# Kernel optimization log

Hardware: AMD Instinct MI355X
Metric: run time of the kernel (lower is better)

## Reference

```python
import jax, jax.numpy as jnp
from jax import lax
import numpy as np

N, V, P, WE, PE, H, M = 512, 50000, 50, 100, 25, 256, 100
D = WE + PE  # 125, LSTM layer-0 input


def setup_inputs() -> dict:
    key = jax.random.key(0)
    ks = jax.random.split(key, 16)
    s = 0.05  # keep tanh/sigmoid in linear-ish range
    rn = lambda k, shape: jax.random.normal(k, shape, jnp.float32) * s
    return {
        "word_idx": jax.random.randint(ks[0], (N,), 0, V),
        "pos_idx": jax.random.randint(ks[1], (N,), 0, P),
        "word_emb": rn(ks[2], (V, WE)),
        "pos_emb": rn(ks[3], (P, PE)),
        "Wih0": rn(ks[4], (2, 4 * H, D)),
        "Whh0": rn(ks[5], (2, 4 * H, H)),
        "bih0": rn(ks[6], (2, 4 * H)),
        "bhh0": rn(ks[7], (2, 4 * H)),
        "Wih1": rn(ks[8], (2, 4 * H, 2 * H)),
        "Whh1": rn(ks[9], (2, 4 * H, H)),
        "bih1": rn(ks[10], (2, 4 * H)),
        "bhh1": rn(ks[11], (2, 4 * H)),
        "W1": rn(ks[12], (M, 4 * H)),
        "b1": rn(ks[13], (M,)),
        "W2": rn(ks[14], (1, M)),
        "b2": rn(ks[15], (1,)),
    }


def _lstm_dir(x, Wih, Whh, bih, bhh, reverse):
    # x: [n, d_in]; PyTorch gate order i, f, g, o
    Hh = Whh.shape[1]
    xp = jnp.flip(x, 0) if reverse else x
    pre = xp @ Wih.T + (bih + bhh)  # [n, 4H], input contribution precomputed

    def step(carry, p):
        h, c = carry
        g = p + h @ Whh.T
        i, f, gg, o = jnp.split(g, 4)
        c = jax.nn.sigmoid(f) * c + jax.nn.sigmoid(i) * jnp.tanh(gg)
        h = jax.nn.sigmoid(o) * jnp.tanh(c)
        return (h, c), h

    init = (jnp.zeros((Hh,), x.dtype), jnp.zeros((Hh,), x.dtype))
    _, hs = lax.scan(step, init, pre)
    return jnp.flip(hs, 0) if reverse else hs


def _bilstm_layer(x, Wih, Whh, bih, bhh):
    fwd = _lstm_dir(x, Wih[0], Whh[0], bih[0], bhh[0], False)
    bwd = _lstm_dir(x, Wih[1], Whh[1], bih[1], bhh[1], True)
    return jnp.concatenate([fwd, bwd], axis=-1)  # [n, 2H]


def reference(word_idx, pos_idx, word_emb, pos_emb,
              Wih0, Whh0, bih0, bhh0, Wih1, Whh1, bih1, bhh1,
              W1, b1, W2, b2):
    # embedding lookup + concat -> [n, D]
    embeds = jnp.concatenate([word_emb[word_idx], pos_emb[pos_idx]], axis=-1)
    h = _bilstm_layer(embeds, Wih0, Whh0, bih0, bhh0)   # [n, 2H]
    h = _bilstm_layer(h, Wih1, Whh1, bih1, bhh1)        # [n, 2H]
    # Pairwise MLP scorer: score[i, j] = W2 @ tanh(W1 @ cat(h_i, h_j) + b1) + b2
    # Split W1 so we never materialize the [n, n, 4H] concat tensor.
    Hd = h.shape[-1]
    a = h @ W1[:, :Hd].T   # [n, M] head part
    b = h @ W1[:, Hd:].T   # [n, M] dep part
    hid = jnp.tanh(a[:, None, :] + b[None, :, :] + b1)  # [n, n, M]
    scores = jnp.einsum('ijm,m->ij', hid, W2[0]) + b2[0]
    return scores
```

## Files before the change

### kernel.cpp

```cpp
#include <hip/hip_runtime.h>
#include <hip/hip_bf16.h>
#include <stdint.h>


typedef _Float16 f16x2 __attribute__((ext_vector_type(2)));

#define SCOPE_AGENT __HIP_MEMORY_SCOPE_AGENT
constexpr uint32_t SENT = 0x7FFF7FFFu;

__device__ __forceinline__ float fdot2f(uint32_t w, uint32_t h, float acc) {
#if __has_builtin(__builtin_amdgcn_fdot2)
  return __builtin_amdgcn_fdot2(__builtin_bit_cast(f16x2, w),
                                __builtin_bit_cast(f16x2, h), acc, false);
#else
  f16x2 a = __builtin_bit_cast(f16x2, w);
  f16x2 b = __builtin_bit_cast(f16x2, h);
  return acc + (float)a.x * (float)b.x + (float)a.y * (float)b.y;
#endif
}

__device__ __forceinline__ float fsigm(float x) { return 1.f / (1.f + __expf(-x)); }
__device__ __forceinline__ float ftanh(float x) {
  float e = __expf(2.f * x);
  return 1.f - 2.f / (e + 1.f);
}

constexpr size_t ALN(size_t x) { return (x + 1023) & ~(size_t)1023; }
constexpr size_t O_EX    = 0;
constexpr size_t SZ_EX   = 4ull * 512 * 128 * 4;
constexpr size_t O_WPK   = ALN(O_EX + SZ_EX);
constexpr size_t SZ_WPK  = 4ull * 128 * 1024 * 4;
constexpr size_t O_X0    = ALN(O_WPK + SZ_WPK);
constexpr size_t SZ_X0   = 512ull * 125 * 4;
constexpr size_t O_WTIH0 = ALN(O_X0 + SZ_X0);
constexpr size_t SZ_WTIH0 = 2ull * 128 * 1024 * 4;
constexpr size_t O_WTIH1 = ALN(O_WTIH0 + SZ_WTIH0);
constexpr size_t SZ_WTIH1 = 2ull * 512 * 1024 * 4;
constexpr size_t O_WTA   = ALN(O_WTIH1 + SZ_WTIH1);
constexpr size_t SZ_WTAB = 512ull * 100 * 4;
constexpr size_t O_WTB   = ALN(O_WTA + SZ_WTAB);
constexpr size_t O_PRE0  = ALN(O_WTB + SZ_WTAB);
constexpr size_t SZ_PRE  = 2ull * 512 * 1024 * 4;
constexpr size_t O_PRE1  = ALN(O_PRE0 + SZ_PRE);
constexpr size_t O_H0    = ALN(O_PRE1 + SZ_PRE);
constexpr size_t SZ_H    = 512ull * 512 * 4;
constexpr size_t O_H1    = ALN(O_H0 + SZ_H);
constexpr size_t O_AM    = ALN(O_H1 + SZ_H);
constexpr size_t O_BT    = ALN(O_AM + SZ_WTAB);


__global__ void k_init_ex(uint32_t* __restrict__ ex) {
  ex[(size_t)blockIdx.x * 256 + threadIdx.x] = SENT;
}

__global__ void k_embed(const int* __restrict__ wi, const int* __restrict__ pi,
                        const float* __restrict__ we, const float* __restrict__ pe,
                        float* __restrict__ x0) {
  int i = blockIdx.x, k = threadIdx.x;
  if (k < 100)      x0[i * 125 + k] = we[(size_t)wi[i] * 100 + k];
  else if (k < 125) x0[i * 125 + k] = pe[(size_t)pi[i] * 25 + (k - 100)];
}

__global__ void k_transpose(const float* __restrict__ src, int srcRows, int srcCols,
                            int colOff, int colCnt, int dstRows, float* __restrict__ dst) {
  __shared__ float tile[32][33];
  int k0 = blockIdx.x * 32, m0 = blockIdx.y * 32;
  int tx = threadIdx.x, ty = threadIdx.y;
#pragma unroll
  for (int i = 0; i < 4; i++) {
    int m = m0 + ty + i * 8, k = k0 + tx;
    float v = 0.f;
    if (m < srcRows && k < colCnt) v = src[(size_t)m * srcCols + colOff + k];
    tile[ty + i * 8][tx] = v;
  }
  __syncthreads();
#pragma unroll
  for (int i = 0; i < 4; i++) {
    int k = k0 + ty + i * 8, m = m0 + tx;
    if (k < dstRows && m < srcRows) dst[(size_t)k * srcRows + m] = tile[tx][ty + i * 8];
  }
}

__global__ void k_packwhh(const float* __restrict__ whh0, const float* __restrict__ whh1,
                          uint32_t* __restrict__ wpk) {
  int ld = blockIdx.x;
  int kp = blockIdx.y;
  int o  = threadIdx.x;
  const float* W = (ld < 2) ? (whh0 + (size_t)ld * 1024 * 256)
                            : (whh1 + (size_t)(ld - 2) * 1024 * 256);
  int b = o >> 9, t = o & 511;
  int gate = t >> 7, u = t & 127;
  int R = gate * 256 + b * 128 + u;
  f16x2 p;
  p.x = (_Float16)W[(size_t)R * 256 + 2 * kp];
  p.y = (_Float16)W[(size_t)R * 256 + 2 * kp + 1];
  wpk[(size_t)ld * 131072 + (size_t)(kp >> 2) * 4096 + (size_t)o * 4 + (kp & 3)] =
      __builtin_bit_cast(uint32_t, p);
}

__global__ __launch_bounds__(256) void k_gemm(
    const float* __restrict__ X, const float* __restrict__ WT,
    const float* __restrict__ bias1, const float* __restrict__ bias2,
    float* __restrict__ out, int Mm, int Nn, int Kpad, int Kreal, int ldx,
    int flipX, int outT) {
  __shared__ float XS[32][64];
  int tid = threadIdx.x;
  int cl = tid & 63, rg = tid >> 6;
  int col = blockIdx.y * 64 + cl;
  int colr = (col < Nn) ? col : (Nn - 1);
  int row0 = blockIdx.x * 32;
  float acc[8];
#pragma unroll
  for (int r = 0; r < 8; r++) acc[r] = 0.f;
  for (int k0 = 0; k0 < Kpad; k0 += 64) {
#pragma unroll
    for (int ii = 0; ii < 8; ii++) {
      int idx = ii * 256 + tid;
      int r = idx >> 6, kk = idx & 63;
      int gr = row0 + r;
      int xr = flipX ? (Mm - 1 - gr) : gr;
      int k = k0 + kk;
      XS[r][kk] = (k < Kreal) ? X[(size_t)xr * ldx + k] : 0.f;
    }
    __syncthreads();
#pragma unroll 4
    for (int kk = 0; kk < 64; kk++) {
      float w = WT[(size_t)(k0 + kk) * Nn + colr];
#pragma unroll
      for (int r = 0; r < 8; r++) acc[r] += XS[rg * 8 + r][kk] * w;
    }
    __syncthreads();
  }
  if (col < Nn) {
    float bb = (bias1 ? bias1[col] : 0.f) + (bias2 ? bias2[col] : 0.f);
#pragma unroll
    for (int r = 0; r < 8; r++) {
      int gr = row0 + rg * 8 + r;
      float v = acc[r] + bb;
      if (outT) out[(size_t)col * Mm + gr] = v;
      else      out[(size_t)gr * Nn + col] = v;
    }
  }
}

__global__ __launch_bounds__(512, 2) void k_lstm(
    const float* __restrict__ preBase, const uint32_t* __restrict__ wpkL,
    float* __restrict__ hout, uint32_t* __restrict__ exL) {
  int d = blockIdx.x >> 1, b = blockIdx.x & 1;
  int t = threadIdx.x;
  const float* pre = preBase + (size_t)d * 512 * 1024;
  const uint32_t* wsrc = wpkL + (size_t)d * 131072;
  uint32_t* ex = exL + (size_t)d * 512 * 128;

  __shared__ __align__(16) uint32_t h2[128];
  __shared__ __align__(8) float gl[512];

  const uint4* wv = (const uint4*)wsrc;
  const int o = b * 512 + t;
#define WLOAD(i) uint4 W##i = wv[(i) * 1024 + o];
  WLOAD(0)  WLOAD(1)  WLOAD(2)  WLOAD(3)  WLOAD(4)  WLOAD(5)  WLOAD(6)  WLOAD(7)
  WLOAD(8)  WLOAD(9)  WLOAD(10) WLOAD(11) WLOAD(12) WLOAD(13) WLOAD(14) WLOAD(15)
  WLOAD(16) WLOAD(17) WLOAD(18) WLOAD(19) WLOAD(20) WLOAD(21) WLOAD(22) WLOAD(23)
  WLOAD(24) WLOAD(25) WLOAD(26) WLOAD(27) WLOAD(28) WLOAD(29) WLOAD(30) WLOAD(31)
#undef WLOAD
#define WPIN(i) asm volatile("" : "+v"(W##i.x), "+v"(W##i.y), "+v"(W##i.z), "+v"(W##i.w));
  WPIN(0)  WPIN(1)  WPIN(2)  WPIN(3)  WPIN(4)  WPIN(5)  WPIN(6)  WPIN(7)
  WPIN(8)  WPIN(9)  WPIN(10) WPIN(11) WPIN(12) WPIN(13) WPIN(14) WPIN(15)
  WPIN(16) WPIN(17) WPIN(18) WPIN(19) WPIN(20) WPIN(21) WPIN(22) WPIN(23)
  WPIN(24) WPIN(25) WPIN(26) WPIN(27) WPIN(28) WPIN(29) WPIN(30) WPIN(31)
#undef WPIN

  if (t < 128) h2[t] = 0u;
  float c0 = 0.f, c1 = 0.f;
  const int gate = t >> 7, u = t & 127;
  const int RR = gate * 256 + b * 128 + u;
  __syncthreads();

  float pcur = pre[RR];
  for (int s = 0; s < 512; s++) {
    float pnext = (s < 511) ? pre[(size_t)(s + 1) * 1024 + RR] : 0.f;
    float a0 = pcur, a1 = 0.f, a2 = 0.f, a3 = 0.f;
    const uint4* h4 = (const uint4*)h2;
#define DOT(i) { uint4 hv = h4[i];                 \
      a0 = fdot2f(W##i.x, hv.x, a0);               \
      a1 = fdot2f(W##i.y, hv.y, a1);               \
      a2 = fdot2f(W##i.z, hv.z, a2);               \
      a3 = fdot2f(W##i.w, hv.w, a3); }
    DOT(0)  DOT(1)  DOT(2)  DOT(3)  DOT(4)  DOT(5)  DOT(6)  DOT(7)
    DOT(8)  DOT(9)  DOT(10) DOT(11) DOT(12) DOT(13) DOT(14) DOT(15)
    DOT(16) DOT(17) DOT(18) DOT(19) DOT(20) DOT(21) DOT(22) DOT(23)
    DOT(24) DOT(25) DOT(26) DOT(27) DOT(28) DOT(29) DOT(30) DOT(31)
#undef DOT
    gl[t] = (a0 + a1) + (a2 + a3);
    __syncthreads();
    if (t < 64) {
      const float2* GL2 = (const float2*)gl;
      float2 gi = GL2[t];
      float2 gf = GL2[64 + t];
      float2 gg = GL2[128 + t];
      float2 go = GL2[192 + t];
      c0 = fsigm(gf.x) * c0 + fsigm(gi.x) * ftanh(gg.x);
      c1 = fsigm(gf.y) * c1 + fsigm(gi.y) * ftanh(gg.y);
      float hA = fsigm(go.x) * ftanh(c0);
      float hB = fsigm(go.y) * ftanh(c1);
      f16x2 p;
      p.x = (_Float16)hA;
      p.y = (_Float16)hB;
      uint32_t pk = __builtin_bit_cast(uint32_t, p);
      __hip_atomic_store(&ex[(size_t)s * 128 + b * 64 + t], pk,
                         __ATOMIC_RELAXED, SCOPE_AGENT);
      h2[b * 64 + t] = pk;
      int pos = (d == 0) ? s : (511 - s);
      *(float2*)&hout[(size_t)pos * 512 + d * 256 + b * 128 + 2 * t] =
          make_float2(hA, hB);
    } else if (t < 128) {
      int tt = t - 64;
      uint32_t q;
      do {
        q = __hip_atomic_load(&ex[(size_t)s * 128 + (b ^ 1) * 64 + tt],
                              __ATOMIC_RELAXED, SCOPE_AGENT);
      } while (__any(q == SENT));
      h2[(b ^ 1) * 64 + tt] = q;
    }
    pcur = pnext;
    __syncthreads();
  }
}

__global__ __launch_bounds__(512) void k_score(
    const float* __restrict__ am, const float* __restrict__ bT,
    const float* __restrict__ W2, const float* __restrict__ b2,
    float* __restrict__ out) {
  int i = blockIdx.x;
  int j = threadIdx.x;
  __shared__ float aL[100], w2L[100];
  if (j < 100) { aL[j] = am[(size_t)i * 100 + j]; w2L[j] = W2[j]; }
  __syncthreads();
  float acc = b2[0];
#pragma unroll 4
  for (int m = 0; m < 100; m++)
    acc += w2L[m] * ftanh(aL[m] + bT[(size_t)m * 512 + j]);
  out[(size_t)i * 512 + j] = acc;
}

extern "C" void kernel_launch(void* const* d_in, const int* in_sizes, int n_in,
                              void* d_out, int out_size, void* d_ws, size_t ws_size,
                              hipStream_t stream) {
  const int*   wi   = (const int*)d_in[0];
  const int*   pi   = (const int*)d_in[1];
  const float* we   = (const float*)d_in[2];
  const float* pe   = (const float*)d_in[3];
  const float* Wih0 = (const float*)d_in[4];
  const float* Whh0 = (const float*)d_in[5];
  const float* bih0 = (const float*)d_in[6];
  const float* bhh0 = (const float*)d_in[7];
  const float* Wih1 = (const float*)d_in[8];
  const float* Whh1 = (const float*)d_in[9];
  const float* bih1 = (const float*)d_in[10];
  const float* bhh1 = (const float*)d_in[11];
  const float* W1   = (const float*)d_in[12];
  const float* b1   = (const float*)d_in[13];
  const float* W2   = (const float*)d_in[14];
  const float* b2   = (const float*)d_in[15];

  char* ws = (char*)d_ws;
  uint32_t* ex    = (uint32_t*)(ws + O_EX);
  uint32_t* wpk   = (uint32_t*)(ws + O_WPK);
  float* x0    = (float*)(ws + O_X0);
  float* wtih0 = (float*)(ws + O_WTIH0);
  float* wtih1 = (float*)(ws + O_WTIH1);
  float* wta   = (float*)(ws + O_WTA);
  float* wtb   = (float*)(ws + O_WTB);
  float* pre0  = (float*)(ws + O_PRE0);
  float* pre1  = (float*)(ws + O_PRE1);
  float* h0    = (float*)(ws + O_H0);
  float* h1    = (float*)(ws + O_H1);
  float* am    = (float*)(ws + O_AM);
  float* bt    = (float*)(ws + O_BT);
  float* out   = (float*)d_out;

  k_init_ex<<<1024, 256, 0, stream>>>(ex);

  k_embed<<<512, 128, 0, stream>>>(wi, pi, we, pe, x0);

  dim3 tb(32, 8);
  k_transpose<<<dim3(4, 32),  tb, 0, stream>>>(Wih0,              1024, 125, 0,   125, 128, wtih0);
  k_transpose<<<dim3(4, 32),  tb, 0, stream>>>(Wih0 + 1024 * 125, 1024, 125, 0,   125, 128, wtih0 + 128 * 1024);
  k_transpose<<<dim3(16, 32), tb, 0, stream>>>(Wih1,              1024, 512, 0,   512, 512, wtih1);
  k_transpose<<<dim3(16, 32), tb, 0, stream>>>(Wih1 + 1024 * 512, 1024, 512, 0,   512, 512, wtih1 + 512 * 1024);
  k_transpose<<<dim3(16, 4),  tb, 0, stream>>>(W1,                100, 1024, 0,   512, 512, wta);
  k_transpose<<<dim3(16, 4),  tb, 0, stream>>>(W1,                100, 1024, 512, 512, 512, wtb);

  k_packwhh<<<dim3(4, 128), 1024, 0, stream>>>(Whh0, Whh1, wpk);

  for (int d = 0; d < 2; d++)
    k_gemm<<<dim3(16, 16), 256, 0, stream>>>(x0, wtih0 + (size_t)d * 128 * 1024,
        bih0 + d * 1024, bhh0 + d * 1024, pre0 + (size_t)d * 512 * 1024,
        512, 1024, 128, 125, 125, d, 0);

  k_lstm<<<4, 512, 0, stream>>>(pre0, wpk, h0, ex);

  for (int d = 0; d < 2; d++)
    k_gemm<<<dim3(16, 16), 256, 0, stream>>>(h0, wtih1 + (size_t)d * 512 * 1024,
        bih1 + d * 1024, bhh1 + d * 1024, pre1 + (size_t)d * 512 * 1024,
        512, 1024, 512, 512, 512, d, 0);

  k_lstm<<<4, 512, 0, stream>>>(pre1, wpk + 2 * 131072, h1, ex + 2ull * 512 * 128);

  k_gemm<<<dim3(16, 2), 256, 0, stream>>>(h1, wta, b1, nullptr, am, 512, 100, 512, 512, 512, 0, 0);
  k_gemm<<<dim3(16, 2), 256, 0, stream>>>(h1, wtb, nullptr, nullptr, bt, 512, 100, 512, 512, 512, 0, 1);

  k_score<<<512, 512, 0, stream>>>(am, bt, W2, b2, out);
}
```

Before: 2.735 ms.

## Split LSTM recurrent dot-product K dimension across two half-blocks of 1024 threads

```diff
diff --git a/kernel.cpp b/kernel.cpp
--- a/kernel.cpp
+++ b/kernel.cpp
@@ -19,6 +19,13 @@
 #endif
 }
 
+__device__ __forceinline__ uint32_t packpair(float x, float y) {
+  f16x2 p;
+  p.x = (_Float16)x;
+  p.y = (_Float16)y;
+  return __builtin_bit_cast(uint32_t, p);
+}
+
 __device__ __forceinline__ float fsigm(float x) { return 1.f / (1.f + __expf(-x)); }
 __device__ __forceinline__ float ftanh(float x) {
   float e = __expf(2.f * x);
@@ -29,7 +36,7 @@
 constexpr size_t O_EX    = 0;
 constexpr size_t SZ_EX   = 4ull * 512 * 128 * 4;
 constexpr size_t O_WPK   = ALN(O_EX + SZ_EX);
-constexpr size_t SZ_WPK  = 4ull * 128 * 1024 * 4;
+constexpr size_t SZ_WPK  = 4ull * 16 * 2048 * 16;
 constexpr size_t O_X0    = ALN(O_WPK + SZ_WPK);
 constexpr size_t SZ_X0   = 512ull * 125 * 4;
 constexpr size_t O_WTIH0 = ALN(O_X0 + SZ_X0);
@@ -84,18 +91,22 @@
 __global__ void k_packwhh(const float* __restrict__ whh0, const float* __restrict__ whh1,
                           uint32_t* __restrict__ wpk) {
   int ld = blockIdx.x;
-  int kp = blockIdx.y;
-  int o  = threadIdx.x;
+  int c  = blockIdx.y;
+  int o  = blockIdx.z * 1024 + threadIdx.x;
   const float* W = (ld < 2) ? (whh0 + (size_t)ld * 1024 * 256)
                             : (whh1 + (size_t)(ld - 2) * 1024 * 256);
-  int b = o >> 9, t = o & 511;
-  int gate = t >> 7, u = t & 127;
+  int b = o >> 10, t = o & 1023;
+  int hi = t >> 9, tr = t & 511;
+  int gate = tr >> 7, u = tr & 127;
   int R = gate * 256 + b * 128 + u;
-  f16x2 p;
-  p.x = (_Float16)W[(size_t)R * 256 + 2 * kp];
-  p.y = (_Float16)W[(size_t)R * 256 + 2 * kp + 1];
-  wpk[(size_t)ld * 131072 + (size_t)(kp >> 2) * 4096 + (size_t)o * 4 + (kp & 3)] =
-      __builtin_bit_cast(uint32_t, p);
+  int khalf = hi ? (b ^ 1) : b;
+  const float* src = W + (size_t)R * 256 + khalf * 128 + c * 8;
+  uint4 outv;
+  outv.x = packpair(src[0], src[1]);
+  outv.y = packpair(src[2], src[3]);
+  outv.z = packpair(src[4], src[5]);
+  outv.w = packpair(src[6], src[7]);
+  ((uint4*)wpk)[(size_t)ld * 32768 + (size_t)c * 2048 + o] = outv;
 }
 
 __global__ __launch_bounds__(256) void k_gemm(
@@ -143,70 +154,67 @@
   }
 }
 
-__global__ __launch_bounds__(512, 2) void k_lstm(
+__global__ __launch_bounds__(1024) void k_lstm(
     const float* __restrict__ preBase, const uint32_t* __restrict__ wpkL,
     float* __restrict__ hout, uint32_t* __restrict__ exL) {
   int d = blockIdx.x >> 1, b = blockIdx.x & 1;
   int t = threadIdx.x;
+  int tr = t & 511, hi = t >> 9;
   const float* pre = preBase + (size_t)d * 512 * 1024;
-  const uint32_t* wsrc = wpkL + (size_t)d * 131072;
   uint32_t* ex = exL + (size_t)d * 512 * 128;
+  const uint4* wv = (const uint4*)(wpkL + (size_t)d * 131072);
 
   __shared__ __align__(16) uint32_t h2[128];
-  __shared__ __align__(8) float gl[512];
-
-  const uint4* wv = (const uint4*)wsrc;
-  const int o = b * 512 + t;
-#define WLOAD(i) uint4 W##i = wv[(i) * 1024 + o];
+  __shared__ __align__(8) float shp[1024];
+
+  const int o = b * 1024 + t;
+  const int khalf = hi ? (b ^ 1) : b;
+
+#define WLOAD(i) uint4 W##i = wv[(i) * 2048 + o];
   WLOAD(0)  WLOAD(1)  WLOAD(2)  WLOAD(3)  WLOAD(4)  WLOAD(5)  WLOAD(6)  WLOAD(7)
   WLOAD(8)  WLOAD(9)  WLOAD(10) WLOAD(11) WLOAD(12) WLOAD(13) WLOAD(14) WLOAD(15)
-  WLOAD(16) WLOAD(17) WLOAD(18) WLOAD(19) WLOAD(20) WLOAD(21) WLOAD(22) WLOAD(23)
-  WLOAD(24) WLOAD(25) WLOAD(26) WLOAD(27) WLOAD(28) WLOAD(29) WLOAD(30) WLOAD(31)
 #undef WLOAD
 #define WPIN(i) asm volatile("" : "+v"(W##i.x), "+v"(W##i.y), "+v"(W##i.z), "+v"(W##i.w));
   WPIN(0)  WPIN(1)  WPIN(2)  WPIN(3)  WPIN(4)  WPIN(5)  WPIN(6)  WPIN(7)
   WPIN(8)  WPIN(9)  WPIN(10) WPIN(11) WPIN(12) WPIN(13) WPIN(14) WPIN(15)
-  WPIN(16) WPIN(17) WPIN(18) WPIN(19) WPIN(20) WPIN(21) WPIN(22) WPIN(23)
-  WPIN(24) WPIN(25) WPIN(26) WPIN(27) WPIN(28) WPIN(29) WPIN(30) WPIN(31)
 #undef WPIN
 
   if (t < 128) h2[t] = 0u;
   float c0 = 0.f, c1 = 0.f;
-  const int gate = t >> 7, u = t & 127;
+  const int gate = tr >> 7, u = tr & 127;
   const int RR = gate * 256 + b * 128 + u;
+  float pcur = (t < 512) ? pre[RR] : 0.f;
   __syncthreads();
 
-  float pcur = pre[RR];
   for (int s = 0; s < 512; s++) {
-    float pnext = (s < 511) ? pre[(size_t)(s + 1) * 1024 + RR] : 0.f;
+    float pnext = (t < 512 && s < 511) ? pre[(size_t)(s + 1) * 1024 + RR] : 0.f;
     float a0 = pcur, a1 = 0.f, a2 = 0.f, a3 = 0.f;
-    const uint4* h4 = (const uint4*)h2;
-#define DOT(i) { uint4 hv = h4[i];                 \
+    const uint4* hb = ((const uint4*)h2) + khalf * 16;
+#define DOT(i) { uint4 hv = hb[i];                 \
       a0 = fdot2f(W##i.x, hv.x, a0);               \
       a1 = fdot2f(W##i.y, hv.y, a1);               \
       a2 = fdot2f(W##i.z, hv.z, a2);               \
       a3 = fdot2f(W##i.w, hv.w, a3); }
     DOT(0)  DOT(1)  DOT(2)  DOT(3)  DOT(4)  DOT(5)  DOT(6)  DOT(7)
     DOT(8)  DOT(9)  DOT(10) DOT(11) DOT(12) DOT(13) DOT(14) DOT(15)
-    DOT(16) DOT(17) DOT(18) DOT(19) DOT(20) DOT(21) DOT(22) DOT(23)
-    DOT(24) DOT(25) DOT(26) DOT(27) DOT(28) DOT(29) DOT(30) DOT(31)
 #undef DOT
-    gl[t] = (a0 + a1) + (a2 + a3);
+    shp[t] = (a0 + a1) + (a2 + a3);
     __syncthreads();
     if (t < 64) {
-      const float2* GL2 = (const float2*)gl;
-      float2 gi = GL2[t];
-      float2 gf = GL2[64 + t];
-      float2 gg = GL2[128 + t];
-      float2 go = GL2[192 + t];
-      c0 = fsigm(gf.x) * c0 + fsigm(gi.x) * ftanh(gg.x);
-      c1 = fsigm(gf.y) * c1 + fsigm(gi.y) * ftanh(gg.y);
-      float hA = fsigm(go.x) * ftanh(c0);
-      float hB = fsigm(go.y) * ftanh(c1);
-      f16x2 p;
-      p.x = (_Float16)hA;
-      p.y = (_Float16)hB;
-      uint32_t pk = __builtin_bit_cast(uint32_t, p);
+      const float2* SP2 = (const float2*)shp;
+      float2 giA = SP2[t],       giB = SP2[256 + t];
+      float2 gfA = SP2[64 + t],  gfB = SP2[320 + t];
+      float2 ggA = SP2[128 + t], ggB = SP2[384 + t];
+      float2 goA = SP2[192 + t], goB = SP2[448 + t];
+      float gi0 = giA.x + giB.x, gi1 = giA.y + giB.y;
+      float gf0 = gfA.x + gfB.x, gf1 = gfA.y + gfB.y;
+      float gg0 = ggA.x + ggB.x, gg1 = ggA.y + ggB.y;
+      float go0 = goA.x + goB.x, go1 = goA.y + goB.y;
+      c0 = fsigm(gf0) * c0 + fsigm(gi0) * ftanh(gg0);
+      c1 = fsigm(gf1) * c1 + fsigm(gi1) * ftanh(gg1);
+      float hA = fsigm(go0) * ftanh(c0);
+      float hB = fsigm(go1) * ftanh(c1);
+      uint32_t pk = packpair(hA, hB);
       __hip_atomic_store(&ex[(size_t)s * 128 + b * 64 + t], pk,
                          __ATOMIC_RELAXED, SCOPE_AGENT);
       h2[b * 64 + t] = pk;
@@ -291,21 +299,21 @@
   k_transpose<<<dim3(16, 4),  tb, 0, stream>>>(W1,                100, 1024, 0,   512, 512, wta);
   k_transpose<<<dim3(16, 4),  tb, 0, stream>>>(W1,                100, 1024, 512, 512, 512, wtb);
 
-  k_packwhh<<<dim3(4, 128), 1024, 0, stream>>>(Whh0, Whh1, wpk);
+  k_packwhh<<<dim3(4, 16, 2), 1024, 0, stream>>>(Whh0, Whh1, wpk);
 
   for (int d = 0; d < 2; d++)
     k_gemm<<<dim3(16, 16), 256, 0, stream>>>(x0, wtih0 + (size_t)d * 128 * 1024,
         bih0 + d * 1024, bhh0 + d * 1024, pre0 + (size_t)d * 512 * 1024,
         512, 1024, 128, 125, 125, d, 0);
 
-  k_lstm<<<4, 512, 0, stream>>>(pre0, wpk, h0, ex);
+  k_lstm<<<4, 1024, 0, stream>>>(pre0, wpk, h0, ex);
 
   for (int d = 0; d < 2; d++)
     k_gemm<<<dim3(16, 16), 256, 0, stream>>>(h0, wtih1 + (size_t)d * 512 * 1024,
         bih1 + d * 1024, bhh1 + d * 1024, pre1 + (size_t)d * 512 * 1024,
         512, 1024, 512, 512, 512, d, 0);
 
-  k_lstm<<<4, 512, 0, stream>>>(pre1, wpk + 2 * 131072, h1, ex + 2ull * 512 * 128);
+  k_lstm<<<4, 1024, 0, stream>>>(pre1, wpk + 2 * 131072, h1, ex + 2ull * 512 * 128);
 
   k_gemm<<<dim3(16, 2), 256, 0, stream>>>(h1, wta, b1, nullptr, am, 512, 100, 512, 512, 512, 0, 0);
   k_gemm<<<dim3(16, 2), 256, 0, stream>>>(h1, wtb, nullptr, nullptr, bt, 512, 100, 512, 512, 512, 0, 1);
```

New measurement: 2.446 ms. 10.6% less time.
